# Optimization experiments

Hardware: AMD Instinct MI355X
Metric: run time of the kernel (lower is better)

The kernel has to match this reference:

```python
import jax, jax.numpy as jnp
import numpy as np

C_Z = 128
C_H = 128
L = 512
EPS = 1e-5


def _layer_norm(x, w, b):
    mu = jnp.mean(x, axis=-1, keepdims=True)
    var = jnp.mean(jnp.square(x - mu), axis=-1, keepdims=True)
    return (x - mu) * jax.lax.rsqrt(var + EPS) * w + b


def setup_inputs() -> dict:
    key = jax.random.key(0)
    ks = jax.random.split(key, 10)
    s_z = 1.0 / np.sqrt(C_Z)
    s_h = 1.0 / np.sqrt(C_H)
    return {
        "z": jax.random.normal(ks[0], (L, L, C_Z), dtype=jnp.float32),
        "pair_mask": jax.random.randint(ks[1], (L, L), 0, 2, dtype=jnp.int32),
        "ln_in_w": jnp.ones((C_Z,), jnp.float32),
        "ln_in_b": jnp.zeros((C_Z,), jnp.float32),
        "ln_out_w": jnp.ones((C_H,), jnp.float32),
        "ln_out_b": jnp.zeros((C_H,), jnp.float32),
        # weights stored [in, out] so forward is x @ W
        "W_proj_a": jax.random.uniform(ks[2], (C_Z, C_H), jnp.float32, -s_z, s_z),
        "W_gate_a": jax.random.uniform(ks[3], (C_Z, C_H), jnp.float32, -s_z, s_z),
        "W_proj_b": jax.random.uniform(ks[4], (C_Z, C_H), jnp.float32, -s_z, s_z),
        "W_gate_b": jax.random.uniform(ks[5], (C_Z, C_H), jnp.float32, -s_z, s_z),
        "W_gate_out": jax.random.uniform(ks[6], (C_Z, C_Z), jnp.float32, -s_z, s_z),
        "W_proj_out": jax.random.uniform(ks[7], (C_H, C_Z), jnp.float32, -s_h, s_h),
    }


def reference(z, pair_mask, ln_in_w, ln_in_b, ln_out_w, ln_out_b,
              W_proj_a, W_gate_a, W_proj_b, W_gate_b, W_gate_out, W_proj_out):
    mask = pair_mask.astype(z.dtype)[..., None]  # [L, L, 1]
    z_ln = _layer_norm(z, ln_in_w, ln_in_b)      # [L, L, c_z]
    a = jax.nn.sigmoid(z_ln @ W_gate_a) * (z_ln @ W_proj_a) * mask  # [L, L, c_h]
    b = jax.nn.sigmoid(z_ln @ W_gate_b) * (z_ln @ W_proj_b) * mask  # [L, L, c_h]
    m = jnp.einsum('ikc,jkc->ijc', a, b)         # channel-batched matmul
    m_ln = _layer_norm(m, ln_out_w, ln_out_b)
    g = jax.nn.sigmoid(z_ln @ W_gate_out)        # [L, L, c_z]
    dz = g * (m_ln @ W_proj_out)
    return dz * mask
```

## Files before the change

kernel.cpp:

```cpp
#include <hip/hip_runtime.h>
#include <stdint.h>

#define LDIM 512
#define LLTOT 262144
#define EPSV 1e-5f

typedef short bf16x8 __attribute__((ext_vector_type(8)));
typedef float f32x4 __attribute__((ext_vector_type(4)));

__device__ __forceinline__ unsigned short f2bf(float f) {
  union { float f; unsigned u; } v; v.f = f;
  unsigned r = v.u + 0x7FFFu + ((v.u >> 16) & 1u);
  return (unsigned short)(r >> 16);
}
__device__ __forceinline__ float bf2f(unsigned short h) {
  union { unsigned u; float f; } v; v.u = ((unsigned)h) << 16;
  return v.f;
}
__device__ __forceinline__ float sigm(float x) { return 1.0f / (1.0f + __expf(-x)); }


__global__ void k_prep(const float* __restrict__ Wpa, const float* __restrict__ Wga,
                       const float* __restrict__ Wpb, const float* __restrict__ Wgb,
                       const float* __restrict__ Wgo, const float* __restrict__ Wpo,
                       unsigned short* __restrict__ Wt) {
  int t = blockIdx.x * blockDim.x + threadIdx.x;
  int mat = t >> 14;
  int rem = t & 16383;
  int o = rem >> 7;
  int c = rem & 127;
  const float* src;
  switch (mat) {
    case 0: src = Wga; break;
    case 1: src = Wpa; break;
    case 2: src = Wgb; break;
    case 3: src = Wpb; break;
    case 4: src = Wgo; break;
    default: src = Wpo; break;
  }
  Wt[mat * 16384 + o * 128 + c] = f2bf(src[c * 128 + o]);
}

__global__ __launch_bounds__(256) void k_proj(const float* __restrict__ z,
                                              const float* __restrict__ lnw,
                                              const float* __restrict__ lnb,
                                              const unsigned short* __restrict__ Wt,
                                              const int* __restrict__ maskp,
                                              unsigned short* __restrict__ a_f,
                                              unsigned short* __restrict__ b_f,
                                              unsigned short* __restrict__ gout) {
  __shared__ unsigned char zbuf[128 * 272];
  __shared__ float maskf[128];
  const int t = threadIdx.x;
  const int bid = blockIdx.x;
  const long r0 = (long)bid * 128;
  const int w = t >> 6, lane = t & 63;
  const int mn = lane & 15, q4 = lane >> 4;
  const int k0 = (bid & 3) * 128;
  const int i16 = bid >> 6;
  const int irem = (bid >> 2) & 15;

  if (t < 128) maskf[t] = (float)maskp[r0 + t];

  const float lw0 = lnw[2 * lane], lw1 = lnw[2 * lane + 1];
  const float lb0 = lnb[2 * lane], lb1 = lnb[2 * lane + 1];
#pragma unroll 2
  for (int rr = 0; rr < 32; rr += 4) {
    float2 v[4];
#pragma unroll
    for (int i = 0; i < 4; ++i)
      v[i] = ((const float2*)(z + (r0 + w * 32 + rr + i) * 128))[lane];
#pragma unroll
    for (int i = 0; i < 4; ++i) {
      float s = v[i].x + v[i].y, q = v[i].x * v[i].x + v[i].y * v[i].y;
#pragma unroll
      for (int off = 32; off; off >>= 1) { s += __shfl_xor(s, off); q += __shfl_xor(q, off); }
      float mu = s * (1.0f / 128.0f);
      float rs = rsqrtf(q * (1.0f / 128.0f) - mu * mu + EPSV);
      ushort2 o;
      o.x = f2bf((v[i].x - mu) * rs * lw0 + lb0);
      o.y = f2bf((v[i].y - mu) * rs * lw1 + lb1);
      ((ushort2*)&zbuf[(w * 32 + rr + i) * 272])[lane] = o;
    }
  }
  __syncthreads();

#pragma unroll 1
  for (int p = 0; p < 2; ++p) {
    const unsigned short* Wg = Wt + (p * 2) * 16384;
    const unsigned short* Wp = Wt + (p * 2 + 1) * 16384;
    unsigned short* dst = p ? b_f : a_f;
    bf16x8 wg[2][4], wp[2][4];
#pragma unroll
    for (int ntl = 0; ntl < 2; ++ntl)
#pragma unroll
      for (int kk = 0; kk < 4; ++kk) {
        const int o = (w * 2 + ntl) * 16 + mn;
        wg[ntl][kk] = *(const bf16x8*)(Wg + o * 128 + kk * 32 + q4 * 8);
        wp[ntl][kk] = *(const bf16x8*)(Wp + o * 128 + kk * 32 + q4 * 8);
      }
#pragma unroll 1
    for (int rg = 0; rg < 8; ++rg) {
      bf16x8 afr[4];
#pragma unroll
      for (int kk = 0; kk < 4; ++kk)
        afr[kk] = *(const bf16x8*)(&zbuf[(rg * 16 + mn) * 272 + kk * 64 + q4 * 16]);
      f32x4 aG[2] = {{0.f,0.f,0.f,0.f},{0.f,0.f,0.f,0.f}};
      f32x4 aP[2] = {{0.f,0.f,0.f,0.f},{0.f,0.f,0.f,0.f}};
#pragma unroll
      for (int kk = 0; kk < 4; ++kk)
#pragma unroll
        for (int ntl = 0; ntl < 2; ++ntl) {
          aG[ntl] = __builtin_amdgcn_mfma_f32_16x16x32_bf16(afr[kk], wg[ntl][kk], aG[ntl], 0, 0, 0);
          aP[ntl] = __builtin_amdgcn_mfma_f32_16x16x32_bf16(afr[kk], wp[ntl][kk], aP[ntl], 0, 0, 0);
        }
      const int rowb = rg * 16 + q4 * 4;
      const int kpos = k0 + rowb;
      const int kc = kpos >> 5;
      const int cell = (irem * 4 + ((kpos >> 3) & 3)) * 16 + (kpos & 7) * 2;
#pragma unroll
      for (int ntl = 0; ntl < 2; ++ntl) {
        const int c = (w * 2 + ntl) * 16 + mn;
        unsigned short hv[4];
#pragma unroll
        for (int r = 0; r < 4; ++r)
          hv[r] = f2bf(sigm(aG[ntl][r]) * aP[ntl][r] * maskf[rowb + r]);
        uint2 pk;
        pk.x = (unsigned)hv[0] | ((unsigned)hv[1] << 16);
        pk.y = (unsigned)hv[2] | ((unsigned)hv[3] << 16);
        *(uint2*)((char*)dst + (long)c * 524288 + kc * 32768 + i16 * 1024 + cell) = pk;
      }
    }
  }

  {
    const unsigned short* Wgp = Wt + 4 * 16384;
    bf16x8 wg[2][4];
#pragma unroll
    for (int ntl = 0; ntl < 2; ++ntl)
#pragma unroll
      for (int kk = 0; kk < 4; ++kk)
        wg[ntl][kk] = *(const bf16x8*)(Wgp + ((w * 2 + ntl) * 16 + mn) * 128 + kk * 32 + q4 * 8);
#pragma unroll 1
    for (int rg = 0; rg < 8; ++rg) {
      bf16x8 afr[4];
#pragma unroll
      for (int kk = 0; kk < 4; ++kk)
        afr[kk] = *(const bf16x8*)(&zbuf[(rg * 16 + mn) * 272 + kk * 64 + q4 * 16]);
      f32x4 aG[2] = {{0.f,0.f,0.f,0.f},{0.f,0.f,0.f,0.f}};
#pragma unroll
      for (int kk = 0; kk < 4; ++kk)
#pragma unroll
        for (int ntl = 0; ntl < 2; ++ntl)
          aG[ntl] = __builtin_amdgcn_mfma_f32_16x16x32_bf16(afr[kk], wg[ntl][kk], aG[ntl], 0, 0, 0);
      const int rowb = rg * 16 + q4 * 4;
#pragma unroll
      for (int ntl = 0; ntl < 2; ++ntl) {
        const int c = (w * 2 + ntl) * 16 + mn;
#pragma unroll
        for (int r = 0; r < 4; ++r)
          gout[(r0 + rowb + r) * 128 + c] = f2bf(sigm(aG[ntl][r]));
      }
    }
  }
}

__global__ __launch_bounds__(256) void k_einsum(const unsigned short* __restrict__ af_g,
                                                const unsigned short* __restrict__ bf_g,
                                                unsigned short* __restrict__ m_t) {
  __shared__ unsigned char shm[36864];
  const int t = threadIdx.x;
  const int w = t >> 6, lane = t & 63;
  const int bid = blockIdx.x;
  const int xcd = bid & 7;
  const int j = bid >> 3;
  const int ch = xcd * 16 + (j >> 4);
  const int tile = j & 15;
  const int ti = tile >> 2, tj = tile & 3;
  const int wr = w >> 1, wc = w & 1;
  const int mn = lane & 15, q4 = lane >> 4;
  const int loff = (mn * 4 + q4) * 16;
  const char* Af = (const char*)af_g + (long)ch * 524288 + (ti * 8 + wr * 4) * 1024 + loff;
  const char* Bf = (const char*)bf_g + (long)ch * 524288 + (tj * 8 + wc * 4) * 1024 + loff;

  f32x4 acc[4][4];
#pragma unroll
  for (int i = 0; i < 4; ++i)
#pragma unroll
    for (int jj = 0; jj < 4; ++jj) acc[i][jj] = (f32x4){0.f, 0.f, 0.f, 0.f};

  bf16x8 afr[2][4], bfr[2][4];
#define LOADFRAG(buf, k32)                                                    \
  {                                                                           \
    _Pragma("unroll")                                                         \
    for (int mt = 0; mt < 4; ++mt)                                            \
      afr[buf][mt] = *(const bf16x8*)(Af + (k32) * 32768 + mt * 1024);        \
    _Pragma("unroll")                                                         \
    for (int nt = 0; nt < 4; ++nt)                                            \
      bfr[buf][nt] = *(const bf16x8*)(Bf + (k32) * 32768 + nt * 1024);        \
  }
#define MFMABLK(buf)                                                          \
  {                                                                           \
    _Pragma("unroll")                                                         \
    for (int mt = 0; mt < 4; ++mt)                                            \
      _Pragma("unroll")                                                       \
      for (int nt = 0; nt < 4; ++nt)                                          \
        acc[mt][nt] = __builtin_amdgcn_mfma_f32_16x16x32_bf16(                \
            afr[buf][mt], bfr[buf][nt], acc[mt][nt], 0, 0, 0);                \
  }

  LOADFRAG(0, 0)
#pragma unroll 1
  for (int k32 = 0; k32 < 14; k32 += 2) {
    LOADFRAG(1, k32 + 1)
    MFMABLK(0)
    LOADFRAG(0, k32 + 2)
    MFMABLK(1)
  }
  LOADFRAG(1, 15)
  MFMABLK(0)
  MFMABLK(1)
#undef LOADFRAG
#undef MFMABLK

  unsigned char* eb = shm + w * 9216;
#pragma unroll
  for (int mt = 0; mt < 4; ++mt)
#pragma unroll
    for (int nt = 0; nt < 4; ++nt)
#pragma unroll
      for (int r = 0; r < 4; ++r) {
        int rl = mt * 16 + q4 * 4 + r;
        int cl = nt * 16 + mn;
        *(unsigned short*)(&eb[rl * 144 + cl * 2]) = f2bf(acc[mt][nt][r]);
      }
  char* Mg = (char*)m_t + (long)ch * 524288 +
             (long)(ti * 128 + wr * 64) * 1024 + (tj * 128 + wc * 64) * 2;
#pragma unroll
  for (int it = 0; it < 8; ++it) {
    int rl = it * 8 + (lane >> 3), cc = lane & 7;
    *(int4*)(Mg + (long)rl * 1024 + cc * 16) = *(const int4*)(&eb[rl * 144 + cc * 16]);
  }
}

__global__ __launch_bounds__(256) void k_out(const unsigned short* __restrict__ m_t,
                                             const unsigned short* __restrict__ gbuf,
                                             const unsigned short* __restrict__ Wt,
                                             const int* __restrict__ maskp,
                                             const float* __restrict__ lnw,
                                             const float* __restrict__ lnb,
                                             float* __restrict__ out) {
  __shared__ unsigned char mln[64 * 272];
  __shared__ float obuf[64 * 132];
  __shared__ float lw[128], lb[128], mk[64];
  const int t = threadIdx.x;
  const long r0 = (long)blockIdx.x * 64;

#pragma unroll
  for (int it = 0; it < 4; ++it) {
    int chunk = it * 256 + t;
    int c = chunk >> 3, cc = chunk & 7;
    int4 rv = *(const int4*)((const char*)m_t + (long)c * 524288 + r0 * 2 + cc * 16);
    const unsigned short* rp = (const unsigned short*)&rv;
#pragma unroll
    for (int e = 0; e < 8; ++e) {
      int er = (e + cc) & 7;
      *(unsigned short*)(&mln[(cc * 8 + er) * 272 + c * 2]) = rp[er];
    }
  }
  if (t < 128) { lw[t] = lnw[t]; lb[t] = lnb[t]; }
  if (t < 64) mk[t] = (float)maskp[r0 + t];
  __syncthreads();

  {
    int row = t >> 2, part = t & 3;
    float xv[32];
    float s = 0.f, q = 0.f;
#pragma unroll
    for (int jj = 0; jj < 16; ++jj) {
      unsigned u = *(const unsigned*)(&mln[row * 272 + part * 64 + jj * 4]);
      float x0 = bf2f((unsigned short)(u & 0xffff));
      float x1 = bf2f((unsigned short)(u >> 16));
      xv[2 * jj] = x0; xv[2 * jj + 1] = x1;
      s += x0 + x1; q += x0 * x0 + x1 * x1;
    }
    s += __shfl_xor(s, 1); q += __shfl_xor(q, 1);
    s += __shfl_xor(s, 2); q += __shfl_xor(q, 2);
    float mu = s * (1.f / 128.f);
    float var = q * (1.f / 128.f) - mu * mu;
    float rs = rsqrtf(var + EPSV);
#pragma unroll
    for (int jj = 0; jj < 16; ++jj) {
      int c = part * 32 + 2 * jj;
      unsigned short h0 = f2bf((xv[2 * jj] - mu) * rs * lw[c] + lb[c]);
      unsigned short h1 = f2bf((xv[2 * jj + 1] - mu) * rs * lw[c + 1] + lb[c + 1]);
      *(unsigned*)(&mln[row * 272 + c * 2]) = (unsigned)h0 | ((unsigned)h1 << 16);
    }
  }
  __syncthreads();

  const int w = t >> 6, lane = t & 63;
  const int mn = lane & 15, q4 = lane >> 4;
  bf16x8 afr[4];
#pragma unroll
  for (int kk = 0; kk < 4; ++kk)
    afr[kk] = *(const bf16x8*)(&mln[(w * 16 + mn) * 272 + kk * 64 + q4 * 16]);
  const unsigned short* Wp = Wt + 5 * 16384;
#pragma unroll 1
  for (int nt = 0; nt < 8; ++nt) {
    f32x4 acc = {0.f, 0.f, 0.f, 0.f};
#pragma unroll
    for (int kk = 0; kk < 4; ++kk) {
      bf16x8 bfr = *(const bf16x8*)(Wp + (nt * 16 + mn) * 128 + kk * 32 + q4 * 8);
      acc = __builtin_amdgcn_mfma_f32_16x16x32_bf16(afr[kk], bfr, acc, 0, 0, 0);
    }
    const int cl = nt * 16 + mn;
#pragma unroll
    for (int r = 0; r < 4; ++r)
      obuf[(w * 16 + q4 * 4 + r) * 132 + cl] = acc[r];
  }
  __syncthreads();

#pragma unroll
  for (int it = 0; it < 8; ++it) {
    int chunk = it * 256 + t;
    int row = chunk >> 5, cc = chunk & 31;
    float4 v = *(const float4*)(&obuf[row * 132 + cc * 4]);
    uint2 gp = *(const uint2*)((const char*)gbuf + (r0 + row) * 256 + cc * 8);
    float mval = mk[row];
    v.x *= bf2f((unsigned short)(gp.x & 0xffff)) * mval;
    v.y *= bf2f((unsigned short)(gp.x >> 16)) * mval;
    v.z *= bf2f((unsigned short)(gp.y & 0xffff)) * mval;
    v.w *= bf2f((unsigned short)(gp.y >> 16)) * mval;
    *(float4*)(out + (r0 + row) * 128 + cc * 4) = v;
  }
}

extern "C" void kernel_launch(void* const* d_in, const int* in_sizes, int n_in,
                              void* d_out, int out_size, void* d_ws, size_t ws_size,
                              hipStream_t stream) {
  const float* z    = (const float*)d_in[0];
  const int* maskp  = (const int*)d_in[1];
  const float* lniw = (const float*)d_in[2];
  const float* lnib = (const float*)d_in[3];
  const float* lnow = (const float*)d_in[4];
  const float* lnob = (const float*)d_in[5];
  const float* Wpa  = (const float*)d_in[6];
  const float* Wga  = (const float*)d_in[7];
  const float* Wpb  = (const float*)d_in[8];
  const float* Wgb  = (const float*)d_in[9];
  const float* Wgo  = (const float*)d_in[10];
  const float* Wpo  = (const float*)d_in[11];
  float* out = (float*)d_out;

  char* ws = (char*)d_ws;
  unsigned short* a_f = (unsigned short*)(ws);
  unsigned short* b_f = (unsigned short*)(ws + 67108864);
  unsigned short* g   = (unsigned short*)(ws + 134217728);
  unsigned short* m_t = (unsigned short*)(ws + 201326592);
  unsigned short* Wt  = (unsigned short*)(ws + 268435456);

  k_prep<<<384, 256, 0, stream>>>(Wpa, Wga, Wpb, Wgb, Wgo, Wpo, Wt);
  k_proj<<<2048, 256, 0, stream>>>(z, lniw, lnib, Wt, maskp, a_f, b_f, g);
  k_einsum<<<2048, 256, 0, stream>>>(a_f, b_f, m_t);
  k_out<<<4096, 256, 0, stream>>>(m_t, g, Wt, maskp, lnow, lnob, out);
}
```

Measured before the change: 529.4 us.

## Stage einsum operands through LDS via global_load_lds and coalesce projection stores

The einsum kernel now loads A/B fragments into double-buffered shared memory using direct global-to-LDS loads, so each 1KB fragment is fetched once per block and shared across waves. Previously each wave loaded its own fragments straight from global memory, which duplicated loads. The projection kernel writes its gated outputs into an LDS staging buffer and then issues coalesced 32-byte stores per channel, replacing scattered 8-byte stores. It also vectorizes the input layernorm to float4 loads with half-wave reductions. These changes add __syncthreads barriers in both kernels and rely on the async LDS load path.

Measured after the change: 507.0 us. -4.2%, faster.

```diff
diff --git a/kernel.cpp b/kernel.cpp
--- a/kernel.cpp
+++ b/kernel.cpp
@@ -7,6 +7,12 @@
 
 typedef short bf16x8 __attribute__((ext_vector_type(8)));
 typedef float f32x4 __attribute__((ext_vector_type(4)));
+typedef __attribute__((address_space(1))) unsigned as1_u32;
+typedef __attribute__((address_space(3))) unsigned as3_u32;
+
+__device__ __forceinline__ void stage16(const void* g, void* l) {
+  __builtin_amdgcn_global_load_lds((as1_u32*)g, (as3_u32*)l, 16, 0, 0);
+}
 
 __device__ __forceinline__ unsigned short f2bf(float f) {
   union { float f; unsigned u; } v; v.f = f;
@@ -49,7 +55,8 @@
                                               unsigned short* __restrict__ a_f,
                                               unsigned short* __restrict__ b_f,
                                               unsigned short* __restrict__ gout) {
-  __shared__ unsigned char zbuf[128 * 272];
+  __shared__ __align__(16) unsigned char zbuf[128 * 272];
+  __shared__ __align__(16) unsigned char stg[128 * 80];
   __shared__ float maskf[128];
   const int t = threadIdx.x;
   const int bid = blockIdx.x;
@@ -62,29 +69,31 @@
 
   if (t < 128) maskf[t] = (float)maskp[r0 + t];
 
-  const float lw0 = lnw[2 * lane], lw1 = lnw[2 * lane + 1];
-  const float lb0 = lnb[2 * lane], lb1 = lnb[2 * lane + 1];
-#pragma unroll 2
-  for (int rr = 0; rr < 32; rr += 4) {
-    float2 v[4];
-#pragma unroll
-    for (int i = 0; i < 4; ++i)
-      v[i] = ((const float2*)(z + (r0 + w * 32 + rr + i) * 128))[lane];
-#pragma unroll
-    for (int i = 0; i < 4; ++i) {
-      float s = v[i].x + v[i].y, q = v[i].x * v[i].x + v[i].y * v[i].y;
-#pragma unroll
-      for (int off = 32; off; off >>= 1) { s += __shfl_xor(s, off); q += __shfl_xor(q, off); }
+  {
+    const int half = lane >> 5, l32 = lane & 31;
+    const float4 lwv = ((const float4*)lnw)[l32];
+    const float4 lbv = ((const float4*)lnb)[l32];
+#pragma unroll 4
+    for (int rr = 0; rr < 32; rr += 2) {
+      const int row = w * 32 + rr + half;
+      float4 v = ((const float4*)(z + (r0 + row) * 128))[l32];
+      float s = (v.x + v.y) + (v.z + v.w);
+      float q = v.x * v.x + v.y * v.y + v.z * v.z + v.w * v.w;
+#pragma unroll
+      for (int off = 16; off; off >>= 1) { s += __shfl_xor(s, off); q += __shfl_xor(q, off); }
       float mu = s * (1.0f / 128.0f);
       float rs = rsqrtf(q * (1.0f / 128.0f) - mu * mu + EPSV);
-      ushort2 o;
-      o.x = f2bf((v[i].x - mu) * rs * lw0 + lb0);
-      o.y = f2bf((v[i].y - mu) * rs * lw1 + lb1);
-      ((ushort2*)&zbuf[(w * 32 + rr + i) * 272])[lane] = o;
-    }
-  }
-  __syncthreads();
-
+      ushort4 o;
+      o.x = f2bf((v.x - mu) * rs * lwv.x + lbv.x);
+      o.y = f2bf((v.y - mu) * rs * lwv.y + lbv.y);
+      o.z = f2bf((v.z - mu) * rs * lwv.z + lbv.z);
+      o.w = f2bf((v.w - mu) * rs * lwv.w + lbv.w);
+      *(ushort4*)(&zbuf[row * 272 + l32 * 8]) = o;
+    }
+  }
+  __syncthreads();
+
+  const int kcbase = k0 >> 5;
 #pragma unroll 1
   for (int p = 0; p < 2; ++p) {
     const unsigned short* Wg = Wt + (p * 2) * 16384;
@@ -115,9 +124,7 @@
           aP[ntl] = __builtin_amdgcn_mfma_f32_16x16x32_bf16(afr[kk], wp[ntl][kk], aP[ntl], 0, 0, 0);
         }
       const int rowb = rg * 16 + q4 * 4;
-      const int kpos = k0 + rowb;
-      const int kc = kpos >> 5;
-      const int cell = (irem * 4 + ((kpos >> 3) & 3)) * 16 + (kpos & 7) * 2;
+      const int kbyte = (rg & 1) * 32 + q4 * 8;
 #pragma unroll
       for (int ntl = 0; ntl < 2; ++ntl) {
         const int c = (w * 2 + ntl) * 16 + mn;
@@ -128,7 +135,18 @@
         uint2 pk;
         pk.x = (unsigned)hv[0] | ((unsigned)hv[1] << 16);
         pk.y = (unsigned)hv[2] | ((unsigned)hv[3] << 16);
-        *(uint2*)((char*)dst + (long)c * 524288 + kc * 32768 + i16 * 1024 + cell) = pk;
+        *(uint2*)(&stg[c * 80 + kbyte]) = pk;
+      }
+      if (rg & 1) {
+        __syncthreads();
+        const int kc = kcbase + (rg >> 1);
+        const int ch2 = t >> 1, off = (t & 1) * 32;
+        char* d = (char*)dst + (long)ch2 * 524288 + (long)kc * 32768 +
+                  i16 * 1024 + irem * 64 + off;
+        const unsigned char* sp = &stg[ch2 * 80 + off];
+        *(int4*)d = *(const int4*)sp;
+        *(int4*)(d + 16) = *(const int4*)(sp + 16);
+        __syncthreads();
       }
     }
   }
@@ -168,7 +186,7 @@
 __global__ __launch_bounds__(256) void k_einsum(const unsigned short* __restrict__ af_g,
                                                 const unsigned short* __restrict__ bf_g,
                                                 unsigned short* __restrict__ m_t) {
-  __shared__ unsigned char shm[36864];
+  __shared__ __align__(16) unsigned char shm[36864];
   const int t = threadIdx.x;
   const int w = t >> 6, lane = t & 63;
   const int bid = blockIdx.x;
@@ -180,8 +198,16 @@
   const int wr = w >> 1, wc = w & 1;
   const int mn = lane & 15, q4 = lane >> 4;
   const int loff = (mn * 4 + q4) * 16;
-  const char* Af = (const char*)af_g + (long)ch * 524288 + (ti * 8 + wr * 4) * 1024 + loff;
-  const char* Bf = (const char*)bf_g + (long)ch * 524288 + (tj * 8 + wc * 4) * 1024 + loff;
+  const long chbase = (long)ch * 524288;
+
+  const char* gsrc[4];
+#pragma unroll
+  for (int u = 0; u < 4; ++u) {
+    const int f = w * 4 + u;
+    gsrc[u] = (f < 8)
+        ? (const char*)af_g + chbase + (long)(ti * 8 + f) * 1024 + lane * 16
+        : (const char*)bf_g + chbase + (long)(tj * 8 + (f - 8)) * 1024 + lane * 16;
+  }
 
   f32x4 acc[4][4];
 #pragma unroll
@@ -189,39 +215,37 @@
 #pragma unroll
     for (int jj = 0; jj < 4; ++jj) acc[i][jj] = (f32x4){0.f, 0.f, 0.f, 0.f};
 
-  bf16x8 afr[2][4], bfr[2][4];
-#define LOADFRAG(buf, k32)                                                    \
-  {                                                                           \
-    _Pragma("unroll")                                                         \
-    for (int mt = 0; mt < 4; ++mt)                                            \
-      afr[buf][mt] = *(const bf16x8*)(Af + (k32) * 32768 + mt * 1024);        \
-    _Pragma("unroll")                                                         \
-    for (int nt = 0; nt < 4; ++nt)                                            \
-      bfr[buf][nt] = *(const bf16x8*)(Bf + (k32) * 32768 + nt * 1024);        \
-  }
-#define MFMABLK(buf)                                                          \
-  {                                                                           \
-    _Pragma("unroll")                                                         \
-    for (int mt = 0; mt < 4; ++mt)                                            \
-      _Pragma("unroll")                                                       \
-      for (int nt = 0; nt < 4; ++nt)                                          \
-        acc[mt][nt] = __builtin_amdgcn_mfma_f32_16x16x32_bf16(                \
-            afr[buf][mt], bfr[buf][nt], acc[mt][nt], 0, 0, 0);                \
-  }
-
-  LOADFRAG(0, 0)
-#pragma unroll 1
-  for (int k32 = 0; k32 < 14; k32 += 2) {
-    LOADFRAG(1, k32 + 1)
-    MFMABLK(0)
-    LOADFRAG(0, k32 + 2)
-    MFMABLK(1)
-  }
-  LOADFRAG(1, 15)
-  MFMABLK(0)
-  MFMABLK(1)
-#undef LOADFRAG
-#undef MFMABLK
+#define STAGE(q, k32)                                                          \
+  {                                                                            \
+    _Pragma("unroll")                                                          \
+    for (int u = 0; u < 4; ++u)                                                \
+      stage16(gsrc[u] + (long)(k32) * 32768,                                   \
+              &shm[(q) * 16384 + (w * 4 + u) * 1024]);                         \
+  }
+
+  int cur = 0;
+  STAGE(0, 0)
+  __syncthreads();
+#pragma unroll 1
+  for (int k32 = 0; k32 < 16; ++k32) {
+    if (k32 < 15) STAGE(cur ^ 1, k32 + 1)
+    bf16x8 afr[4], bfr[4];
+#pragma unroll
+    for (int mt = 0; mt < 4; ++mt)
+      afr[mt] = *(const bf16x8*)(&shm[cur * 16384 + (wr * 4 + mt) * 1024 + loff]);
+#pragma unroll
+    for (int nt = 0; nt < 4; ++nt)
+      bfr[nt] = *(const bf16x8*)(&shm[cur * 16384 + 8192 + (wc * 4 + nt) * 1024 + loff]);
+#pragma unroll
+    for (int mt = 0; mt < 4; ++mt)
+#pragma unroll
+      for (int nt = 0; nt < 4; ++nt)
+        acc[mt][nt] = __builtin_amdgcn_mfma_f32_16x16x32_bf16(
+            afr[mt], bfr[nt], acc[mt][nt], 0, 0, 0);
+    __syncthreads();
+    cur ^= 1;
+  }
+#undef STAGE
 
   unsigned char* eb = shm + w * 9216;
 #pragma unroll
```
